# Kernel tuning notes

Hardware: AMD Instinct MI355X
Metric: run time of the kernel (lower is better)

Reference implementation:

```python
import jax, jax.numpy as jnp
import numpy as np

N_NODES = 50000
N_EDGES = 800000
D = 64
VOCAB = 1000
NUM_ITERS = 2
BN_EPS = 1e-5


def _bn(h, g, b):
    # BatchNorm1d in training mode: batch statistics over the edge dim, biased var
    mu = h.mean(axis=0)
    var = h.var(axis=0)
    return g * (h - mu) * jax.lax.rsqrt(var + BN_EPS) + b


def _edge_agg(x, idx_i, idx_j, W1, b1, g1, be1, W2, b2, g2, be2):
    # gather -> concat -> Linear+BN+ReLU x2 -> scatter-sum to idx_i -> degree norm
    m = jnp.concatenate([x[idx_i], x[idx_j]], axis=1)          # [E, 2D]
    h = jax.nn.relu(_bn(m @ W1 + b1, g1, be1))                  # [E, D]
    h = jax.nn.relu(_bn(h @ W2 + b2, g2, be2))                  # [E, D]
    agg = jax.ops.segment_sum(h, idx_i, num_segments=N_NODES)   # [N, D]
    deg = jax.ops.segment_sum(jnp.ones((idx_i.shape[0],), x.dtype), idx_i,
                              num_segments=N_NODES)
    deg_inv = jnp.where(deg > 0, 1.0 / deg, 0.0)
    return deg_inv[:, None] * agg


def setup_inputs() -> dict:
    key = jax.random.key(0)
    ks = jax.random.split(key, 24)
    s = 0.05
    inp = {
        'nodes': jax.random.randint(ks[0], (N_NODES,), 0, VOCAB),
        'edges': jax.random.randint(ks[1], (2, N_EDGES), 0, N_NODES),
        'emb': jax.random.normal(ks[2], (VOCAB, D), jnp.float32) * s,
        # parent aggregation MLP
        'p_W1': jax.random.normal(ks[3], (2 * D, D), jnp.float32) * s,
        'p_b1': jnp.zeros((D,), jnp.float32),
        'p_g1': jnp.ones((D,), jnp.float32),
        'p_be1': jnp.zeros((D,), jnp.float32),
        'p_W2': jax.random.normal(ks[4], (D, D), jnp.float32) * s,
        'p_b2': jnp.zeros((D,), jnp.float32),
        'p_g2': jnp.ones((D,), jnp.float32),
        'p_be2': jnp.zeros((D,), jnp.float32),
        # child aggregation MLP
        'c_W1': jax.random.normal(ks[5], (2 * D, D), jnp.float32) * s,
        'c_b1': jnp.zeros((D,), jnp.float32),
        'c_g1': jnp.ones((D,), jnp.float32),
        'c_be1': jnp.zeros((D,), jnp.float32),
        'c_W2': jax.random.normal(ks[6], (D, D), jnp.float32) * s,
        'c_b2': jnp.zeros((D,), jnp.float32),
        'c_g2': jnp.ones((D,), jnp.float32),
        'c_be2': jnp.zeros((D,), jnp.float32),
        # final aggregation (dropout = identity, eval semantics)
        'fc_W': jax.random.normal(ks[7], (3 * D, 2 * D), jnp.float32) * s,
        'fc_b': jnp.zeros((2 * D,), jnp.float32),
        'fc2_W': jax.random.normal(ks[8], (2 * D, D), jnp.float32) * s,
        'fc2_b': jnp.zeros((D,), jnp.float32),
        # Conv1d(D, 2D, kernel=1) == Linear D -> 2D
        'conv_W': jax.random.normal(ks[9], (D, 2 * D), jnp.float32) * s,
        'conv_b': jnp.zeros((2 * D,), jnp.float32),
    }
    return inp


def reference(nodes, edges, emb, p_W1, p_b1, p_g1, p_be1, p_W2, p_b2, p_g2, p_be2,
              c_W1, c_b1, c_g1, c_be1, c_W2, c_b2, c_g2, c_be2,
              fc_W, fc_b, fc2_W, fc2_b, conv_W, conv_b):
    src, dst = edges[0], edges[1]
    x = emb[nodes]                                            # [N, D]
    for _ in range(NUM_ITERS):
        # ParentAggregation: flow source_to_target -> x_i = x[dst], x_j = x[src], scatter to dst
        fi = _edge_agg(x, dst, src, p_W1, p_b1, p_g1, p_be1, p_W2, p_b2, p_g2, p_be2)
        # ChildAggregation: flow target_to_source -> x_i = x[src], x_j = x[dst], scatter to src
        fo = _edge_agg(x, src, dst, c_W1, c_b1, c_g1, c_be1, c_W2, c_b2, c_g2, c_be2)
        cat = jnp.concatenate([x, fi, fo], axis=1)            # [N, 3D]
        upd = jax.nn.relu(cat @ fc_W + fc_b) @ fc2_W + fc2_b  # [N, D]
        x = x + upd
    return x @ conv_W + conv_b                                # [N, 2D]
```

## Files before the change

kernel.cpp:

```cpp
#include <hip/hip_runtime.h>

#define NN 50000
#define NE 800000
#define BN_EPS 1e-5f
#define SCAN_T 256
#define SCAN_NB ((NN + SCAN_T - 1) / SCAN_T)

#define BKT_SH 8
#define NBKT ((NN + 255) >> 8)
#define CAP 6144
#define PCH 4096
#define NPB ((NE + PCH - 1) / PCH)

#define ST_SUM1 0
#define ST_SQ1 64
#define ST_CROSS 128
#define ST_SUM2 192
#define ST_SSQ2 256
#define ST_AGG 320

using bf16x8 = __attribute__((ext_vector_type(8))) __bf16;
using bf16x4 = __attribute__((ext_vector_type(4))) __bf16;
using floatx4 = __attribute__((ext_vector_type(4))) float;

// ... 131 lines not shown
      int u = (t >= o) ? sm[t - o] : 0;
      __syncthreads();
      sm[t] += u;
      __syncthreads();
    }
    if (t < SCAN_NB) btot[y * SCAN_NB + t] = sm[t] - v;
    __syncthreads();
  }
}

__global__ void k_scan3(const int* __restrict__ cnt_d, const int* __restrict__ cnt_s,
                        int* __restrict__ off_d, int* __restrict__ off_s,
                        const int* __restrict__ btot, float* __restrict__ dinv_d,
                        float* __restrict__ dinv_s) {
  const int* cnt = blockIdx.y ? cnt_s : cnt_d;
  int* off = blockIdx.y ? off_s : off_d;
  float* dinv = blockIdx.y ? dinv_s : dinv_d;
  int i = blockIdx.x * SCAN_T + threadIdx.x;
  if (i < NN) {
    int incl = off[i];
    int c = cnt[i];
    int o = incl - c + btot[blockIdx.y * SCAN_NB + blockIdx.x];
    off[i] = o;
    dinv[i] = c > 0 ? 1.0f / (float)c : 0.f;
  }
  if (i == NN - 1) off[NN] = NE;
}

__global__ void __launch_bounds__(256) k_fill2(const int* __restrict__ bcur,
                                               const unsigned int* __restrict__ stage,
                                               const int* __restrict__ off_d,
                                               const int* __restrict__ off_s,
                                               unsigned short* __restrict__ jl_d,
                                               unsigned short* __restrict__ jl_s) {
  const int dir = blockIdx.y;
  const int b = blockIdx.x;
  const int* off = dir ? off_s : off_d;
  unsigned short* jl = dir ? jl_s : jl_d;
  const unsigned int* st = stage + (size_t)dir * NBKT * CAP + (size_t)b * CAP;
  __shared__ int lcur[256];
  __shared__ unsigned short ljl[CAP];
  int csr0 = off[b << BKT_SH];
  int n = (b << BKT_SH) + threadIdx.x;
  lcur[threadIdx.x] = (n < NN) ? off[n] - csr0 : 0;
  __syncthreads();
  int sz = bcur[dir * NBKT + b] - b * CAP;
  for (int t = threadIdx.x; t < sz; t += 256) {
    unsigned int v = st[t];
    int p = atomicAdd(&lcur[(v >> 16) - (b << BKT_SH)], 1);
    ljl[p] = (unsigned short)(v & 0xFFFFu);
  }
  __syncthreads();
  for (int t = threadIdx.x; t < sz; t += 256) jl[csr0 + t] = ljl[t];
}

__global__ void __launch_bounds__(256) k_node_xform(
    const float* __restrict__ x, const float* __restrict__ W1,
    __bf16* __restrict__ Ab, __bf16* __restrict__ Bb,
    float* __restrict__ stats, int do_zero) {
  const int lane = threadIdx.x & 63;
  const int wid = threadIdx.x >> 6;
  __shared__ alignas(16) __bf16 xb[4][16 * 72];
  if (do_zero && blockIdx.x == 0)
    for (int t = threadIdx.x; t < 2 * ST_AGG; t += blockDim.x) stats[t] = 0.f;
  bf16x8 wfa[4][2], wfb[4][2];
#pragma unroll
  for (int ct = 0; ct < 4; ++ct)
#pragma unroll
    for (int kb = 0; kb < 2; ++kb) {
      wfa[ct][kb] = load_wfrag(W1, 64, kb, ct, lane);
      wfb[ct][kb] = load_wfrag(W1 + 64 * 64, 64, kb, ct, lane);
    }
  __bf16* vb = xb[wid];
  int wgid = (blockIdx.x * blockDim.x + threadIdx.x) >> 6;
  int nw = (gridDim.x * blockDim.x) >> 6;
  for (int tile = wgid; tile < NN / 16; tile += nw) {
#pragma unroll
    for (int t = 0; t < 16; ++t)
      vb[t * 72 + lane] = (__bf16)x[(tile * 16 + t) * 64 + lane];
    const bf16x8 a0 = *(const bf16x8*)&vb[(lane & 15) * 72 + ((lane >> 4) << 3)];
    const bf16x8 a1 = *(const bf16x8*)&vb[(lane & 15) * 72 + 32 + ((lane >> 4) << 3)];
#pragma unroll
    for (int ct = 0; ct < 4; ++ct) {
      floatx4 aA = {0.f, 0.f, 0.f, 0.f}, aB = {0.f, 0.f, 0.f, 0.f};
      aA = MFMA16(a0, wfa[ct][0], aA);
      aA = MFMA16(a1, wfa[ct][1], aA);
      aB = MFMA16(a0, wfb[ct][0], aB);
      aB = MFMA16(a1, wfb[ct][1], aB);
#pragma unroll
      for (int r = 0; r < 4; ++r) {
        int row = ((lane >> 4) << 2) + r;
        int o = (tile * 16 + row) * 64 + ct * 16 + (lane & 15);
        Ab[o] = (__bf16)aA[r];
        Bb[o] = (__bf16)aB[r];
      }
    }
  }
}

__global__ void __launch_bounds__(256) k_node_stats(
    const __bf16* __restrict__ Ap, const __bf16* __restrict__ Bp,
    const __bf16* __restrict__ Ac, const __bf16* __restrict__ Bc,
    const int* __restrict__ cnt_d, const int* __restrict__ cnt_s,
    float* __restrict__ stats) {
  const int lane = threadIdx.x & 63;
  const int g = lane >> 4, q = lane & 15;
  __shared__ float sacc[256];
  for (int t = threadIdx.x; t < 256; t += blockDim.x) sacc[t] = 0.f;
  __syncthreads();
  float sp[4] = {0, 0, 0, 0}, qp[4] = {0, 0, 0, 0};
  float sc[4] = {0, 0, 0, 0}, qc[4] = {0, 0, 0, 0};
  int wgid = (blockIdx.x * blockDim.x + threadIdx.x) >> 6;
  int nw = (gridDim.x * blockDim.x) >> 6;
  for (int ch = wgid; ch < NN / 4; ch += nw) {
    int n = ch * 4 + g;
    float wd = (float)cnt_d[n];
    float ws = (float)cnt_s[n];
    bf16x4 ap = *(const bf16x4*)(Ap + n * 64 + 4 * q);
    bf16x4 bp = *(const bf16x4*)(Bp + n * 64 + 4 * q);
    bf16x4 ac = *(const bf16x4*)(Ac + n * 64 + 4 * q);
    bf16x4 bc = *(const bf16x4*)(Bc + n * 64 + 4 * q);
#pragma unroll
    for (int k = 0; k < 4; ++k) {
      float a = (float)ap[k], b = (float)bp[k], c = (float)ac[k], d = (float)bc[k];
      sp[k] += wd * a + ws * b;
      qp[k] += wd * a * a + ws * b * b;
      sc[k] += ws * c + wd * d;
      qc[k] += ws * c * c + wd * d * d;
    }
  }
#pragma unroll
  for (int k = 0; k < 4; ++k) {
    sp[k] += __shfl_xor(sp[k], 16); sp[k] += __shfl_xor(sp[k], 32);
    qp[k] += __shfl_xor(qp[k], 16); qp[k] += __shfl_xor(qp[k], 32);
    sc[k] += __shfl_xor(sc[k], 16); sc[k] += __shfl_xor(sc[k], 32);
    qc[k] += __shfl_xor(qc[k], 16); qc[k] += __shfl_xor(qc[k], 32);
  }
  if (lane < 16) {
#pragma unroll
    for (int k = 0; k < 4; ++k) {
      atomicAdd(&sacc[4 * q + k], sp[k]);
      atomicAdd(&sacc[64 + 4 * q + k], qp[k]);
      atomicAdd(&sacc[128 + 4 * q + k], sc[k]);
      atomicAdd(&sacc[192 + 4 * q + k], qc[k]);
    }
  }
  __syncthreads();
  for (int t = threadIdx.x; t < 256; t += blockDim.x) {
    int dstoff = (t < 128) ? t : ST_AGG + (t - 128);
    atomicAdd(&stats[dstoff], sacc[t]);
  }
}

__global__ void __launch_bounds__(256) k_cross(
    const int* __restrict__ src, const int* __restrict__ dst,
    const __bf16* __restrict__ Ap, const __bf16* __restrict__ Bp,
    const __bf16* __restrict__ Ac, const __bf16* __restrict__ Bc,
    float* __restrict__ stats) {
  const int lane = threadIdx.x & 63;
  const int g = lane >> 4, q = lane & 15;
  __shared__ float sacc[128];
  for (int t = threadIdx.x; t < 128; t += blockDim.x) sacc[t] = 0.f;
  __syncthreads();
  float cp[4] = {0, 0, 0, 0}, cc[4] = {0, 0, 0, 0};
  int wgid = (blockIdx.x * blockDim.x + threadIdx.x) >> 6;
  int nw = (gridDim.x * blockDim.x) >> 6;
  for (int ch = wgid; ch < NE / 64; ch += nw) {
    int e0 = ch * 64;
    int s64 = src[e0 + lane];
    int d64 = dst[e0 + lane];
#pragma unroll 4
    for (int t = 0; t < 16; ++t) {
      int u = t * 4 + g;
      int s = __shfl(s64, u);
      int d = __shfl(d64, u);
      bf16x4 ap = *(const bf16x4*)(Ap + d * 64 + 4 * q);
      bf16x4 bp = *(const bf16x4*)(Bp + s * 64 + 4 * q);
      bf16x4 ac = *(const bf16x4*)(Ac + s * 64 + 4 * q);
      bf16x4 bc = *(const bf16x4*)(Bc + d * 64 + 4 * q);
#pragma unroll
      for (int k = 0; k < 4; ++k) {
        cp[k] += (float)ap[k] * (float)bp[k];
        cc[k] += (float)ac[k] * (float)bc[k];
      }
    }
  }
#pragma unroll
  for (int k = 0; k < 4; ++k) {
    cp[k] += __shfl_xor(cp[k], 16); cp[k] += __shfl_xor(cp[k], 32);
    cc[k] += __shfl_xor(cc[k], 16); cc[k] += __shfl_xor(cc[k], 32);
  }
  if (lane < 16) {
#pragma unroll
    for (int k = 0; k < 4; ++k) {
      atomicAdd(&sacc[4 * q + k], cp[k]);
      atomicAdd(&sacc[64 + 4 * q + k], cc[k]);
    }
  }
  __syncthreads();
  for (int t = threadIdx.x; t < 128; t += blockDim.x) {
    int dstoff = (t < 64) ? (ST_CROSS + t) : (ST_AGG + ST_CROSS + (t - 64));
    atomicAdd(&stats[dstoff], sacc[t]);
  }
}

__global__ void __launch_bounds__(256) k_edge_stats2(
    const int* __restrict__ src, const int* __restrict__ dst,
    const __bf16* __restrict__ Ap, const __bf16* __restrict__ Bp,
    const __bf16* __restrict__ Ac, const __bf16* __restrict__ Bc,
    const float* __restrict__ pg1, const float* __restrict__ pbe1,
    const float* __restrict__ cg1, const float* __restrict__ cbe1,
    const float* __restrict__ pW2, const float* __restrict__ cW2,
    float* __restrict__ stats) {
  const int lane = threadIdx.x & 63;
  const int wid = threadIdx.x >> 6;
  const int g = lane >> 4, q = lane & 15;
  __shared__ alignas(16) __bf16 vbuf[4][2][16 * 72];
  __shared__ float sred[256];
  float s1p[4], t1p[4], s1c[4], t1c[4];
#pragma unroll
  for (int k = 0; k < 4; ++k) {
    int c = 4 * q + k;
    float mu = stats[ST_SUM1 + c] * (1.f / NE);
    float var = (stats[ST_SQ1 + c] + 2.f * stats[ST_CROSS + c]) * (1.f / NE) - mu * mu;
    float s = pg1[c] * rsqrtf(var + BN_EPS);
    s1p[k] = s;
    t1p[k] = pbe1[c] - mu * s;
    mu = stats[ST_AGG + ST_SUM1 + c] * (1.f / NE);
    var = (stats[ST_AGG + ST_SQ1 + c] + 2.f * stats[ST_AGG + ST_CROSS + c]) * (1.f / NE) - mu * mu;
    s = cg1[c] * rsqrtf(var + BN_EPS);
    s1c[k] = s;
    t1c[k] = cbe1[c] - mu * s;
  }
  bf16x8 wfp[4][2], wfc[4][2];
#pragma unroll
  for (int ct = 0; ct < 4; ++ct)
#pragma unroll
    for (int kb = 0; kb < 2; ++kb) {
      wfp[ct][kb] = load_wfrag(pW2, 64, kb, ct, lane);
      wfc[ct][kb] = load_wfrag(cW2, 64, kb, ct, lane);
    }
  float sump[4] = {0, 0, 0, 0}, ssqp[4] = {0, 0, 0, 0};
  float sumc[4] = {0, 0, 0, 0}, ssqc[4] = {0, 0, 0, 0};
  __bf16* vbp = vbuf[wid][0];
  __bf16* vbc = vbuf[wid][1];
  int wgid = (blockIdx.x * blockDim.x + threadIdx.x) >> 6;
  int nw = (gridDim.x * blockDim.x) >> 6;
  for (int tile = wgid; tile < NE / 16; tile += nw) {
    int e0 = tile * 16;
    int s16 = src[e0 + q];
    int d16 = dst[e0 + q];
#pragma unroll
    for (int t = 0; t < 4; ++t) {
      int et = t * 4 + g;
      int s = __shfl(s16, et);
      int d = __shfl(d16, et);
      bf16x4 ap = *(const bf16x4*)(Ap + (size_t)d * 64 + 4 * q);
      bf16x4 bp = *(const bf16x4*)(Bp + (size_t)s * 64 + 4 * q);
      bf16x4 ac = *(const bf16x4*)(Ac + (size_t)s * 64 + 4 * q);
      bf16x4 bc = *(const bf16x4*)(Bc + (size_t)d * 64 + 4 * q);
      bf16x4 vp4, vc4;
#pragma unroll
      for (int k = 0; k < 4; ++k) {
        vp4[k] = (__bf16)fmaxf(s1p[k] * ((float)ap[k] + (float)bp[k]) + t1p[k], 0.f);
        vc4[k] = (__bf16)fmaxf(s1c[k] * ((float)ac[k] + (float)bc[k]) + t1c[k], 0.f);
      }
      *(bf16x4*)&vbp[et * 72 + 4 * q] = vp4;
      *(bf16x4*)&vbc[et * 72 + 4 * q] = vc4;
    }
    const bf16x8 a0p = *(const bf16x8*)&vbp[q * 72 + g * 8];
    const bf16x8 a1p = *(const bf16x8*)&vbp[q * 72 + 32 + g * 8];
    const bf16x8 a0c = *(const bf16x8*)&vbc[q * 72 + g * 8];
    const bf16x8 a1c = *(const bf16x8*)&vbc[q * 72 + 32 + g * 8];
#pragma unroll
    for (int ct = 0; ct < 4; ++ct) {
      floatx4 accp = {0.f, 0.f, 0.f, 0.f}, accc = {0.f, 0.f, 0.f, 0.f};
      accp = MFMA16(a0p, wfp[ct][0], accp);
      accp = MFMA16(a1p, wfp[ct][1], accp);
      accc = MFMA16(a0c, wfc[ct][0], accc);
      accc = MFMA16(a1c, wfc[ct][1], accc);
#pragma unroll
      for (int r = 0; r < 4; ++r) {
        float hp = accp[r], hc = accc[r];
        sump[ct] += hp;
        ssqp[ct] += hp * hp;
        sumc[ct] += hc;
        ssqc[ct] += hc * hc;
      }
    }
  }
  for (int t = threadIdx.x; t < 256; t += blockDim.x) sred[t] = 0.f;
  __syncthreads();
#pragma unroll
  for (int ct = 0; ct < 4; ++ct) {
    atomicAdd(&sred[ct * 16 + q], sump[ct]);
    atomicAdd(&sred[64 + ct * 16 + q], ssqp[ct]);
    atomicAdd(&sred[128 + ct * 16 + q], sumc[ct]);
    atomicAdd(&sred[192 + ct * 16 + q], ssqc[ct]);
  }
  __syncthreads();
  for (int t = threadIdx.x; t < 256; t += blockDim.x) {
    int dstoff;
    if (t < 64) dstoff = ST_SUM2 + t;
    else if (t < 128) dstoff = ST_SSQ2 + (t - 64);
    else if (t < 192) dstoff = ST_AGG + ST_SUM2 + (t - 128);
    else dstoff = ST_AGG + ST_SSQ2 + (t - 192);
    atomicAdd(&stats[dstoff], sred[t]);
  }
}

__global__ void __launch_bounds__(256) k_scatter_fused(
    const int* __restrict__ off, const float* __restrict__ dinv,
    const unsigned short* __restrict__ jl, const __bf16* __restrict__ A_,
    const __bf16* __restrict__ B_, const float* __restrict__ g1,
    const float* __restrict__ be1, const float* __restrict__ g2,
    const float* __restrict__ be2, const float* __restrict__ W2,
    const float* __restrict__ stats, int sbase, float* __restrict__ outb) {
  const int lane = threadIdx.x & 63;
  const int wid = threadIdx.x >> 6;
  const int g = lane >> 4, q = lane & 15;
  __shared__ alignas(16) __bf16 vbuf[4][16 * 72];
  float s1v[4], t1v[4];
#pragma unroll
  for (int k = 0; k < 4; ++k) {
    int c = 4 * q + k;
    float mu = stats[sbase + ST_SUM1 + c] * (1.f / NE);
    float var = (stats[sbase + ST_SQ1 + c] + 2.f * stats[sbase + ST_CROSS + c]) * (1.f / NE) - mu * mu;
    float s = g1[c] * rsqrtf(var + BN_EPS);
    s1v[k] = s;
    t1v[k] = be1[c] - mu * s;
  }
  float s2v[4], t2v[4];
#pragma unroll
  for (int ct = 0; ct < 4; ++ct) {
    int c = ct * 16 + q;
    float mu = stats[sbase + ST_SUM2 + c] * (1.f / NE);
    float var = stats[sbase + ST_SSQ2 + c] * (1.f / NE) - mu * mu;
    float s = g2[c] * rsqrtf(var + BN_EPS);
    s2v[ct] = s;
    t2v[ct] = be2[c] - mu * s;
  }
  bf16x8 wf[4][2];
#pragma unroll
  for (int ct = 0; ct < 4; ++ct)
#pragma unroll
    for (int kb = 0; kb < 2; ++kb) wf[ct][kb] = load_wfrag(W2, 64, kb, ct, lane);
  __bf16* vb = vbuf[wid];
  int wgid = (blockIdx.x * blockDim.x + threadIdx.x) >> 6;
  int nw = (gridDim.x * blockDim.x) >> 6;
  for (int n = wgid; n < NN; n += nw) {
    int p0 = off[n], p1 = off[n + 1];
    bf16x4 a4 = *(const bf16x4*)(A_ + (size_t)n * 64 + 4 * q);
    float ha[4];
#pragma unroll
    for (int k = 0; k < 4; ++k) ha[k] = (float)a4[k];
    float oacc[4] = {0.f, 0.f, 0.f, 0.f};
    for (int pt = p0; pt < p1; pt += 16) {
      int m = p1 - pt;
      if (m > 16) m = 16;
      int jj = (lane < m) ? (int)jl[pt + lane] : 0;
#pragma unroll
      for (int t = 0; t < 4; ++t) {
        int et = t * 4 + g;
        int j = __shfl(jj, et);
        bf16x4 b4 = *(const bf16x4*)(B_ + (size_t)j * 64 + 4 * q);
        bf16x4 v4;
#pragma unroll
        for (int k = 0; k < 4; ++k)
          v4[k] = (__bf16)fmaxf(s1v[k] * (ha[k] + (float)b4[k]) + t1v[k], 0.f);
        *(bf16x4*)&vb[et * 72 + 4 * q] = v4;
      }
      const bf16x8 a0 = *(const bf16x8*)&vb[q * 72 + g * 8];
      const bf16x8 a1 = *(const bf16x8*)&vb[q * 72 + 32 + g * 8];
#pragma unroll
      for (int ct = 0; ct < 4; ++ct) {
        floatx4 acc = {0.f, 0.f, 0.f, 0.f};
        acc = MFMA16(a0, wf[ct][0], acc);
        acc = MFMA16(a1, wf[ct][1], acc);
#pragma unroll
        for (int r = 0; r < 4; ++r)
          if (g * 4 + r < m) oacc[ct] += fmaxf(s2v[ct] * acc[r] + t2v[ct], 0.f);
      }
    }
#pragma unroll
    for (int ct = 0; ct < 4; ++ct) {
      oacc[ct] += __shfl_xor(oacc[ct], 16);
      oacc[ct] += __shfl_xor(oacc[ct], 32);
    }
    float val = (g == 0) ? oacc[0] : (g == 1) ? oacc[1] : (g == 2) ? oacc[2] : oacc[3];
    outb[(size_t)n * 64 + lane] = dinv[n] * val;
  }
}

__global__ void __launch_bounds__(256) k_node_update(
    float* __restrict__ x, const float* __restrict__ fi, const float* __restrict__ fo,
    const float* __restrict__ fcW, const float* __restrict__ fcb,
    const float* __restrict__ fc2W, const float* __restrict__ fc2b) {
  const int lane = threadIdx.x & 63;
  const int wid = threadIdx.x >> 6;
  __shared__ alignas(16) __bf16 cat[16 * 200];
  __shared__ alignas(16) __bf16 v2[16 * 136];
  bf16x8 wf1[2][6];
#pragma unroll
  for (int c = 0; c < 2; ++c) {
    int ct = 2 * wid + c;
#pragma unroll
    for (int kb = 0; kb < 6; ++kb) wf1[c][kb] = load_wfrag(fcW, 128, kb, ct, lane);
  }
  bf16x8 wf2[4];
#pragma unroll
  for (int kb = 0; kb < 4; ++kb) wf2[kb] = load_wfrag(fc2W, 64, kb, wid, lane);
  float fcbv[2];
#pragma unroll
  for (int c = 0; c < 2; ++c) fcbv[c] = fcb[(2 * wid + c) * 16 + (lane & 15)];
  float fc2bv = fc2b[wid * 16 + (lane & 15)];

  for (int tile = blockIdx.x; tile < NN / 16; tile += gridDim.x) {
#pragma unroll
    for (int r = 0; r < 4; ++r) {
      int rr = wid * 4 + r;
      int n = tile * 16 + rr;
      cat[rr * 200 + lane] = (__bf16)x[n * 64 + lane];
      cat[rr * 200 + 64 + lane] = (__bf16)fi[n * 64 + lane];
      cat[rr * 200 + 128 + lane] = (__bf16)fo[n * 64 + lane];
    }
    __syncthreads();
    floatx4 acc0 = {0.f, 0.f, 0.f, 0.f}, acc1 = {0.f, 0.f, 0.f, 0.f};
#pragma unroll
    for (int kb = 0; kb < 6; ++kb) {
      bf16x8 af = *(const bf16x8*)&cat[(lane & 15) * 200 + kb * 32 + ((lane >> 4) << 3)];
      acc0 = MFMA16(af, wf1[0][kb], acc0);
      acc1 = MFMA16(af, wf1[1][kb], acc1);
    }
#pragma unroll
    for (int r = 0; r < 4; ++r) {
      int row = ((lane >> 4) << 2) + r;
      v2[row * 136 + (2 * wid) * 16 + (lane & 15)] = (__bf16)fmaxf(acc0[r] + fcbv[0], 0.f);
      v2[row * 136 + (2 * wid + 1) * 16 + (lane & 15)] = (__bf16)fmaxf(acc1[r] + fcbv[1], 0.f);
    }
    __syncthreads();
    floatx4 a2 = {0.f, 0.f, 0.f, 0.f};
#pragma unroll
    for (int kb = 0; kb < 4; ++kb) {
      bf16x8 af = *(const bf16x8*)&v2[(lane & 15) * 136 + kb * 32 + ((lane >> 4) << 3)];
      a2 = MFMA16(af, wf2[kb], a2);
    }
#pragma unroll
    for (int r = 0; r < 4; ++r) {
      int row = ((lane >> 4) << 2) + r;
      int n = tile * 16 + row;
      x[n * 64 + wid * 16 + (lane & 15)] += a2[r] + fc2bv;
    }
    __syncthreads();
  }
}

__global__ void __launch_bounds__(256) k_conv(const float* __restrict__ x,
                                              const float* __restrict__ convW,
                                              const float* __restrict__ convb,
                                              float* __restrict__ out) {
  const int lane = threadIdx.x & 63;
  int wgid = (blockIdx.x * blockDim.x + threadIdx.x) >> 6;
  int nw = (gridDim.x * blockDim.x) >> 6;
  int half = wgid & 1;
  int col = half * 64 + lane;
  float wreg[64];
#pragma unroll
  for (int k = 0; k < 64; ++k) wreg[k] = convW[k * 128 + col];
  float bv = convb[col];
  for (int n = (wgid >> 1); n < NN; n += (nw >> 1)) {
    float xv = x[n * 64 + lane];
    float acc = bv;
#pragma unroll
    for (int k = 0; k < 64; ++k) acc += __shfl(xv, k) * wreg[k];
    out[(size_t)n * 128 + col] = acc;
  }
}

extern "C" void kernel_launch(void* const* d_in, const int* in_sizes, int n_in,
                              void* d_out, int out_size, void* d_ws, size_t ws_size,
                              hipStream_t stream) {
  const int* nodes = (const int*)d_in[0];
  const int* edges = (const int*)d_in[1];
  const int* src = edges;
  const int* dst = edges + NE;
  const float* emb = (const float*)d_in[2];
  const float* pW1 = (const float*)d_in[3];
  const float* pg1 = (const float*)d_in[5];
  const float* pbe1 = (const float*)d_in[6];
  const float* pW2 = (const float*)d_in[7];
  const float* pg2 = (const float*)d_in[9];
  const float* pbe2 = (const float*)d_in[10];
  const float* cW1 = (const float*)d_in[11];
  const float* cg1 = (const float*)d_in[13];
  const float* cbe1 = (const float*)d_in[14];
  const float* cW2 = (const float*)d_in[15];
  const float* cg2 = (const float*)d_in[17];
  const float* cbe2 = (const float*)d_in[18];
  const float* fcW = (const float*)d_in[19];
  const float* fcb = (const float*)d_in[20];
  const float* fc2W = (const float*)d_in[21];
  const float* fc2b = (const float*)d_in[22];
  const float* convW = (const float*)d_in[23];
  const float* convb = (const float*)d_in[24];
  float* out = (float*)d_out;

  char* w = (char*)d_ws;
  auto alloc = [&](size_t bytes) {
    char* p = w;
    w += (bytes + 255) & ~(size_t)255;
    return p;
  };
  float* x = (float*)alloc((size_t)NN * 64 * 4);
  __bf16* Ap = (__bf16*)alloc((size_t)NN * 64 * 2);
  __bf16* Bp = (__bf16*)alloc((size_t)NN * 64 * 2);
  __bf16* Ac = (__bf16*)alloc((size_t)NN * 64 * 2);
  __bf16* Bc = (__bf16*)alloc((size_t)NN * 64 * 2);
  float* fi = (float*)alloc((size_t)NN * 64 * 4);
  float* fo = (float*)alloc((size_t)NN * 64 * 4);
  unsigned short* jl_d = (unsigned short*)alloc((size_t)NE * 2);
  unsigned short* jl_s = (unsigned short*)alloc((size_t)NE * 2);
  int* off_d = (int*)alloc((size_t)(NN + 1) * 4);
  int* off_s = (int*)alloc((size_t)(NN + 1) * 4);
  int* cnt_d = (int*)alloc((size_t)NN * 4);
  int* cnt_s = (int*)alloc((size_t)NN * 4);
  float* dinv_d = (float*)alloc((size_t)NN * 4);
  float* dinv_s = (float*)alloc((size_t)NN * 4);
  float* stats = (float*)alloc(2 * ST_AGG * 4);
  int* btot = (int*)alloc(2 * SCAN_NB * 4);
  int* bcur = (int*)alloc((size_t)2 * NBKT * 4);
  unsigned int* stage = (unsigned int*)alloc((size_t)2 * NBKT * CAP * 4);

  k_setup<<<1024, 256, 0, stream>>>(nodes, emb, x, bcur);
  k_part<<<dim3(NPB, 2), 256, 0, stream>>>(src, dst, bcur, stage);
  k_count<<<dim3(NBKT, 2), 256, 0, stream>>>(bcur, stage, cnt_d, cnt_s);
  k_scan1<<<dim3(SCAN_NB, 2), SCAN_T, 0, stream>>>(cnt_d, cnt_s, off_d, off_s, btot);
  k_scan2<<<1, SCAN_T, 0, stream>>>(btot);
  k_scan3<<<dim3(SCAN_NB, 2), SCAN_T, 0, stream>>>(cnt_d, cnt_s, off_d, off_s, btot,
                                                   dinv_d, dinv_s);
  k_fill2<<<dim3(NBKT, 2), 256, 0, stream>>>(bcur, stage, off_d, off_s, jl_d, jl_s);

  for (int it = 0; it < 2; ++it) {
    k_node_xform<<<784, 256, 0, stream>>>(x, pW1, Ap, Bp, stats, 1);
    k_node_xform<<<784, 256, 0, stream>>>(x, cW1, Ac, Bc, stats, 0);
    k_node_stats<<<256, 256, 0, stream>>>(Ap, Bp, Ac, Bc, cnt_d, cnt_s, stats);
    k_cross<<<1024, 256, 0, stream>>>(src, dst, Ap, Bp, Ac, Bc, stats);
    k_edge_stats2<<<2048, 256, 0, stream>>>(src, dst, Ap, Bp, Ac, Bc, pg1, pbe1,
                                            cg1, cbe1, pW2, cW2, stats);
    k_scatter_fused<<<2048, 256, 0, stream>>>(off_d, dinv_d, jl_d, Ap, Bp, pg1, pbe1,
                                              pg2, pbe2, pW2, stats, 0, fi);
    k_scatter_fused<<<2048, 256, 0, stream>>>(off_s, dinv_s, jl_s, Ac, Bc, cg1, cbe1,
                                              cg2, cbe2, cW2, stats, ST_AGG, fo);
    k_node_update<<<3125, 256, 0, stream>>>(x, fi, fo, fcW, fcb, fc2W, fc2b);
  }
  k_conv<<<2048, 256, 0, stream>>>(x, convW, convb, out);
}
```

Before: 927.5 us.

## Materialize second-layer edge activations instead of recomputing them in the scatter pass

When the workspace is large enough, each aggregation direction now runs a CSR-ordered edge MLP kernel that computes layer-2 pre-BN activations once. It stores them in bf16 and accumulates their BN statistics, and a second kernel then applies BN2/ReLU and does the degree-normalized segment sum. This removes the old pattern where the stats pass and the scatter pass each recomputed the gather plus layer-2 matmul. In exchange it writes and reads a 100MB bf16 buffer per direction and adds bf16 rounding of pre-BN values. The old path is kept as a fallback when the workspace is too small.

Result: slower. 1.024 ms (+10.4%).

```diff
diff --git a/kernel.cpp b/kernel.cpp
--- a/kernel.cpp
+++ b/kernel.cpp
@@ -356,6 +356,141 @@
   for (int t = threadIdx.x; t < 128; t += blockDim.x) {
     int dstoff = (t < 64) ? (ST_CROSS + t) : (ST_AGG + ST_CROSS + (t - 64));
     atomicAdd(&stats[dstoff], sacc[t]);
+  }
+}
+
+__global__ void __launch_bounds__(256) k_edge_mlp(
+    const int* __restrict__ off, const unsigned short* __restrict__ jl,
+    const __bf16* __restrict__ A_, const __bf16* __restrict__ B_,
+    const float* __restrict__ g1, const float* __restrict__ be1,
+    const float* __restrict__ W2, float* __restrict__ stats, int sbase,
+    __bf16* __restrict__ hseq) {
+  const int lane = threadIdx.x & 63;
+  const int wid = threadIdx.x >> 6;
+  const int g = lane >> 4, q = lane & 15;
+  __shared__ alignas(16) __bf16 vbuf[4][16 * 72];
+  __shared__ float sred[128];
+  float s1v[4], t1v[4];
+#pragma unroll
+  for (int k = 0; k < 4; ++k) {
+    int c = 4 * q + k;
+    float mu = stats[sbase + ST_SUM1 + c] * (1.f / NE);
+    float var = (stats[sbase + ST_SQ1 + c] + 2.f * stats[sbase + ST_CROSS + c]) * (1.f / NE) - mu * mu;
+    float s = g1[c] * rsqrtf(var + BN_EPS);
+    s1v[k] = s;
+    t1v[k] = be1[c] - mu * s;
+  }
+  bf16x8 wf[4][2];
+#pragma unroll
+  for (int ct = 0; ct < 4; ++ct)
+#pragma unroll
+    for (int kb = 0; kb < 2; ++kb) wf[ct][kb] = load_wfrag(W2, 64, kb, ct, lane);
+  float sum2[4] = {0.f, 0.f, 0.f, 0.f}, ssq2[4] = {0.f, 0.f, 0.f, 0.f};
+  __bf16* vb = vbuf[wid];
+  int wgid = (blockIdx.x * blockDim.x + threadIdx.x) >> 6;
+  int nw = (gridDim.x * blockDim.x) >> 6;
+  for (int n = wgid; n < NN; n += nw) {
+    int p0 = off[n], p1 = off[n + 1];
+    bf16x4 a4 = *(const bf16x4*)(A_ + (size_t)n * 64 + 4 * q);
+    float ha[4];
+#pragma unroll
+    for (int k = 0; k < 4; ++k) ha[k] = (float)a4[k];
+    for (int pt = p0; pt < p1; pt += 16) {
+      int m = p1 - pt;
+      if (m > 16) m = 16;
+      int jj = (lane < m) ? (int)jl[pt + lane] : 0;
+#pragma unroll
+      for (int t = 0; t < 4; ++t) {
+        int et = t * 4 + g;
+        int j = __shfl(jj, et);
+        bf16x4 b4 = *(const bf16x4*)(B_ + (size_t)j * 64 + 4 * q);
+        bf16x4 v4;
+#pragma unroll
+        for (int k = 0; k < 4; ++k)
+          v4[k] = (__bf16)fmaxf(s1v[k] * (ha[k] + (float)b4[k]) + t1v[k], 0.f);
+        *(bf16x4*)&vb[et * 72 + 4 * q] = v4;
+      }
+      const bf16x8 a0 = *(const bf16x8*)&vb[q * 72 + g * 8];
+      const bf16x8 a1 = *(const bf16x8*)&vb[q * 72 + 32 + g * 8];
+      floatx4 acc[4];
+#pragma unroll
+      for (int ct = 0; ct < 4; ++ct) {
+        floatx4 a = {0.f, 0.f, 0.f, 0.f};
+        a = MFMA16(a0, wf[ct][0], a);
+        a = MFMA16(a1, wf[ct][1], a);
+        acc[ct] = a;
+      }
+#pragma unroll
+      for (int ct = 0; ct < 4; ++ct)
+#pragma unroll
+        for (int r = 0; r < 4; ++r) {
+          if (g * 4 + r < m) {
+            float h = acc[ct][r];
+            sum2[ct] += h;
+            ssq2[ct] += h * h;
+            hseq[(size_t)(pt + g * 4 + r) * 64 + ct * 16 + q] = (__bf16)h;
+          }
+        }
+    }
+  }
+  for (int t = threadIdx.x; t < 128; t += blockDim.x) sred[t] = 0.f;
+  __syncthreads();
+#pragma unroll
+  for (int ct = 0; ct < 4; ++ct) {
+    atomicAdd(&sred[ct * 16 + q], sum2[ct]);
+    atomicAdd(&sred[64 + ct * 16 + q], ssq2[ct]);
+  }
+  __syncthreads();
+  for (int t = threadIdx.x; t < 128; t += blockDim.x) {
+    int dstoff = (t < 64) ? (ST_SUM2 + t) : (ST_SSQ2 + (t - 64));
+    atomicAdd(&stats[sbase + dstoff], sred[t]);
+  }
+}
+
+__global__ void __launch_bounds__(256) k_bn2_apply(
+    const int* __restrict__ off, const float* __restrict__ dinv,
+    const __bf16* __restrict__ hseq, const float* __restrict__ g2,
+    const float* __restrict__ be2, const float* __restrict__ stats, int sbase,
+    float* __restrict__ outb) {
+  const int lane = threadIdx.x & 63;
+  const int c0 = (lane & 7) * 8;
+  float s2[8], t2[8];
+#pragma unroll
+  for (int j = 0; j < 8; ++j) {
+    int c = c0 + j;
+    float mu = stats[sbase + ST_SUM2 + c] * (1.f / NE);
+    float var = stats[sbase + ST_SSQ2 + c] * (1.f / NE) - mu * mu;
+    float s = g2[c] * rsqrtf(var + BN_EPS);
+    s2[j] = s;
+    t2[j] = be2[c] - mu * s;
+  }
+  int wgid = (blockIdx.x * blockDim.x + threadIdx.x) >> 6;
+  int nw = (gridDim.x * blockDim.x) >> 6;
+  for (int n = wgid; n < NN; n += nw) {
+    int p0 = off[n], p1 = off[n + 1];
+    float acc[8] = {0.f, 0.f, 0.f, 0.f, 0.f, 0.f, 0.f, 0.f};
+    for (int pt = p0; pt < p1; pt += 8) {
+      int r = pt + (lane >> 3);
+      if (r < p1) {
+        bf16x8 h = *(const bf16x8*)(hseq + (size_t)r * 64 + c0);
+#pragma unroll
+        for (int j = 0; j < 8; ++j)
+          acc[j] += fmaxf(s2[j] * (float)h[j] + t2[j], 0.f);
+      }
+    }
+#pragma unroll
+    for (int j = 0; j < 8; ++j) {
+      acc[j] += __shfl_xor(acc[j], 8);
+      acc[j] += __shfl_xor(acc[j], 16);
+      acc[j] += __shfl_xor(acc[j], 32);
+    }
+    if (lane < 8) {
+      float dv = dinv[n];
+      floatx4 o0 = {dv * acc[0], dv * acc[1], dv * acc[2], dv * acc[3]};
+      floatx4 o1 = {dv * acc[4], dv * acc[5], dv * acc[6], dv * acc[7]};
+      *(floatx4*)&outb[(size_t)n * 64 + lane * 8] = o0;
+      *(floatx4*)&outb[(size_t)n * 64 + lane * 8 + 4] = o1;
+    }
   }
 }
 
@@ -685,6 +820,8 @@
   int* btot = (int*)alloc(2 * SCAN_NB * 4);
   int* bcur = (int*)alloc((size_t)2 * NBKT * 4);
   unsigned int* stage = (unsigned int*)alloc((size_t)2 * NBKT * CAP * 4);
+  __bf16* hseq = (__bf16*)alloc((size_t)NE * 64 * 2);
+  const bool big_ws = ((size_t)(w - (char*)d_ws) <= ws_size);
 
   k_setup<<<1024, 256, 0, stream>>>(nodes, emb, x, bcur);
   k_part<<<dim3(NPB, 2), 256, 0, stream>>>(src, dst, bcur, stage);
@@ -700,12 +837,23 @@
     k_node_xform<<<784, 256, 0, stream>>>(x, cW1, Ac, Bc, stats, 0);
     k_node_stats<<<256, 256, 0, stream>>>(Ap, Bp, Ac, Bc, cnt_d, cnt_s, stats);
     k_cross<<<1024, 256, 0, stream>>>(src, dst, Ap, Bp, Ac, Bc, stats);
-    k_edge_stats2<<<2048, 256, 0, stream>>>(src, dst, Ap, Bp, Ac, Bc, pg1, pbe1,
-                                            cg1, cbe1, pW2, cW2, stats);
-    k_scatter_fused<<<2048, 256, 0, stream>>>(off_d, dinv_d, jl_d, Ap, Bp, pg1, pbe1,
-                                              pg2, pbe2, pW2, stats, 0, fi);
-    k_scatter_fused<<<2048, 256, 0, stream>>>(off_s, dinv_s, jl_s, Ac, Bc, cg1, cbe1,
-                                              cg2, cbe2, cW2, stats, ST_AGG, fo);
+    if (big_ws) {
+      k_edge_mlp<<<2048, 256, 0, stream>>>(off_d, jl_d, Ap, Bp, pg1, pbe1, pW2,
+                                           stats, 0, hseq);
+      k_bn2_apply<<<1024, 256, 0, stream>>>(off_d, dinv_d, hseq, pg2, pbe2, stats,
+                                            0, fi);
+      k_edge_mlp<<<2048, 256, 0, stream>>>(off_s, jl_s, Ac, Bc, cg1, cbe1, cW2,
+                                           stats, ST_AGG, hseq);
+      k_bn2_apply<<<1024, 256, 0, stream>>>(off_s, dinv_s, hseq, cg2, cbe2, stats,
+                                            ST_AGG, fo);
+    } else {
+      k_edge_stats2<<<2048, 256, 0, stream>>>(src, dst, Ap, Bp, Ac, Bc, pg1, pbe1,
+                                              cg1, cbe1, pW2, cW2, stats);
+      k_scatter_fused<<<2048, 256, 0, stream>>>(off_d, dinv_d, jl_d, Ap, Bp, pg1, pbe1,
+                                                pg2, pbe2, pW2, stats, 0, fi);
+      k_scatter_fused<<<2048, 256, 0, stream>>>(off_s, dinv_s, jl_s, Ac, Bc, cg1, cbe1,
+                                                cg2, cbe2, cW2, stats, ST_AGG, fo);
+    }
     k_node_update<<<3125, 256, 0, stream>>>(x, fi, fo, fcW, fcb, fc2W, fc2b);
   }
   k_conv<<<2048, 256, 0, stream>>>(x, convW, convb, out);
```

## Widen edge gathers to 16-byte loads and process two nodes per wave in scatter

Applied to the files above, without the earlier changes.

In the edge-stats and scatter kernels, each lane now gathers 8 bf16 values (16 bytes) of a row instead of 4, so 8 lanes cover a 64-wide row and one wave handles 8 edges per load step. The scatter kernel also processes two destination nodes per wave iteration, with separate LDS staging buffers and interleaved MFMAs. The goal is fewer, wider memory requests and more independent loads in flight to hide gather latency. The cost is higher register use, and when the two nodes have unequal degree the wave does masked work for the shorter one.

Result: no change. 939.3 us (+1.3%).

```diff
diff --git a/kernel.cpp b/kernel.cpp
--- a/kernel.cpp
+++ b/kernel.cpp
@@ -370,12 +370,14 @@
   const int lane = threadIdx.x & 63;
   const int wid = threadIdx.x >> 6;
   const int g = lane >> 4, q = lane & 15;
+  const int c8 = lane & 7;
+  const int e8 = lane >> 3;
   __shared__ alignas(16) __bf16 vbuf[4][2][16 * 72];
   __shared__ float sred[256];
-  float s1p[4], t1p[4], s1c[4], t1c[4];
-#pragma unroll
-  for (int k = 0; k < 4; ++k) {
-    int c = 4 * q + k;
+  float s1p[8], t1p[8], s1c[8], t1c[8];
+#pragma unroll
+  for (int k = 0; k < 8; ++k) {
+    int c = c8 * 8 + k;
     float mu = stats[ST_SUM1 + c] * (1.f / NE);
     float var = (stats[ST_SQ1 + c] + 2.f * stats[ST_CROSS + c]) * (1.f / NE) - mu * mu;
     float s = pg1[c] * rsqrtf(var + BN_EPS);
@@ -403,25 +405,25 @@
   int nw = (gridDim.x * blockDim.x) >> 6;
   for (int tile = wgid; tile < NE / 16; tile += nw) {
     int e0 = tile * 16;
-    int s16 = src[e0 + q];
-    int d16 = dst[e0 + q];
-#pragma unroll
-    for (int t = 0; t < 4; ++t) {
-      int et = t * 4 + g;
-      int s = __shfl(s16, et);
-      int d = __shfl(d16, et);
-      bf16x4 ap = *(const bf16x4*)(Ap + (size_t)d * 64 + 4 * q);
-      bf16x4 bp = *(const bf16x4*)(Bp + (size_t)s * 64 + 4 * q);
-      bf16x4 ac = *(const bf16x4*)(Ac + (size_t)s * 64 + 4 * q);
-      bf16x4 bc = *(const bf16x4*)(Bc + (size_t)d * 64 + 4 * q);
-      bf16x4 vp4, vc4;
-#pragma unroll
-      for (int k = 0; k < 4; ++k) {
-        vp4[k] = (__bf16)fmaxf(s1p[k] * ((float)ap[k] + (float)bp[k]) + t1p[k], 0.f);
-        vc4[k] = (__bf16)fmaxf(s1c[k] * ((float)ac[k] + (float)bc[k]) + t1c[k], 0.f);
+    int sv = src[e0 + q];
+    int dv = dst[e0 + q];
+#pragma unroll
+    for (int r = 0; r < 2; ++r) {
+      int ee = r * 8 + e8;
+      int s = __shfl(sv, ee);
+      int d = __shfl(dv, ee);
+      bf16x8 ap = *(const bf16x8*)(Ap + (size_t)d * 64 + c8 * 8);
+      bf16x8 bp = *(const bf16x8*)(Bp + (size_t)s * 64 + c8 * 8);
+      bf16x8 ac = *(const bf16x8*)(Ac + (size_t)s * 64 + c8 * 8);
+      bf16x8 bc = *(const bf16x8*)(Bc + (size_t)d * 64 + c8 * 8);
+      bf16x8 vp, vc;
+#pragma unroll
+      for (int k = 0; k < 8; ++k) {
+        vp[k] = (__bf16)fmaxf(s1p[k] * ((float)ap[k] + (float)bp[k]) + t1p[k], 0.f);
+        vc[k] = (__bf16)fmaxf(s1c[k] * ((float)ac[k] + (float)bc[k]) + t1c[k], 0.f);
       }
-      *(bf16x4*)&vbp[et * 72 + 4 * q] = vp4;
-      *(bf16x4*)&vbc[et * 72 + 4 * q] = vc4;
+      *(bf16x8*)&vbp[ee * 72 + c8 * 8] = vp;
+      *(bf16x8*)&vbc[ee * 72 + c8 * 8] = vc;
     }
     const bf16x8 a0p = *(const bf16x8*)&vbp[q * 72 + g * 8];
     const bf16x8 a1p = *(const bf16x8*)&vbp[q * 72 + 32 + g * 8];
@@ -474,11 +476,13 @@
   const int lane = threadIdx.x & 63;
   const int wid = threadIdx.x >> 6;
   const int g = lane >> 4, q = lane & 15;
-  __shared__ alignas(16) __bf16 vbuf[4][16 * 72];
-  float s1v[4], t1v[4];
-#pragma unroll
-  for (int k = 0; k < 4; ++k) {
-    int c = 4 * q + k;
+  const int c8 = lane & 7;
+  const int e8 = lane >> 3;
+  __shared__ alignas(16) __bf16 vbuf[4][2][16 * 72];
+  float s1v[8], t1v[8];
+#pragma unroll
+  for (int k = 0; k < 8; ++k) {
+    int c = c8 * 8 + k;
     float mu = stats[sbase + ST_SUM1 + c] * (1.f / NE);
     float var = (stats[sbase + ST_SQ1 + c] + 2.f * stats[sbase + ST_CROSS + c]) * (1.f / NE) - mu * mu;
     float s = g1[c] * rsqrtf(var + BN_EPS);
@@ -500,50 +504,77 @@
   for (int ct = 0; ct < 4; ++ct)
 #pragma unroll
     for (int kb = 0; kb < 2; ++kb) wf[ct][kb] = load_wfrag(W2, 64, kb, ct, lane);
-  __bf16* vb = vbuf[wid];
+  __bf16* vb0 = vbuf[wid][0];
+  __bf16* vb1 = vbuf[wid][1];
   int wgid = (blockIdx.x * blockDim.x + threadIdx.x) >> 6;
   int nw = (gridDim.x * blockDim.x) >> 6;
-  for (int n = wgid; n < NN; n += nw) {
-    int p0 = off[n], p1 = off[n + 1];
-    bf16x4 a4 = *(const bf16x4*)(A_ + (size_t)n * 64 + 4 * q);
-    float ha[4];
-#pragma unroll
-    for (int k = 0; k < 4; ++k) ha[k] = (float)a4[k];
-    float oacc[4] = {0.f, 0.f, 0.f, 0.f};
-    for (int pt = p0; pt < p1; pt += 16) {
-      int m = p1 - pt;
-      if (m > 16) m = 16;
-      int jj = (lane < m) ? (int)jl[pt + lane] : 0;
-#pragma unroll
-      for (int t = 0; t < 4; ++t) {
-        int et = t * 4 + g;
-        int j = __shfl(jj, et);
-        bf16x4 b4 = *(const bf16x4*)(B_ + (size_t)j * 64 + 4 * q);
-        bf16x4 v4;
-#pragma unroll
-        for (int k = 0; k < 4; ++k)
-          v4[k] = (__bf16)fmaxf(s1v[k] * (ha[k] + (float)b4[k]) + t1v[k], 0.f);
-        *(bf16x4*)&vb[et * 72 + 4 * q] = v4;
+  for (int pp = wgid; pp < NN / 2; pp += nw) {
+    int n0 = 2 * pp, n1 = n0 + 1;
+    int p00 = off[n0], p01 = off[n1], p11 = off[n1 + 1];
+    int d0 = p01 - p00, d1 = p11 - p01;
+    bf16x8 a80 = *(const bf16x8*)(A_ + (size_t)n0 * 64 + c8 * 8);
+    bf16x8 a81 = *(const bf16x8*)(A_ + (size_t)n1 * 64 + c8 * 8);
+    float ha0[8], ha1[8];
+#pragma unroll
+    for (int k = 0; k < 8; ++k) { ha0[k] = (float)a80[k]; ha1[k] = (float)a81[k]; }
+    float oacc0[4] = {0.f, 0.f, 0.f, 0.f};
+    float oacc1[4] = {0.f, 0.f, 0.f, 0.f};
+    int T0 = (d0 + 15) >> 4, T1 = (d1 + 15) >> 4;
+    int T = (T0 > T1) ? T0 : T1;
+    for (int tt = 0; tt < T; ++tt) {
+      int b = tt * 16;
+      int m0 = d0 - b; if (m0 > 16) m0 = 16;
+      int m1 = d1 - b; if (m1 > 16) m1 = 16;
+      int jj0 = (lane < m0) ? (int)jl[p00 + b + lane] : 0;
+      int jj1 = (lane < m1) ? (int)jl[p01 + b + lane] : 0;
+      int j00 = __shfl(jj0, e8), j01 = __shfl(jj0, 8 + e8);
+      int j10 = __shfl(jj1, e8), j11 = __shfl(jj1, 8 + e8);
+      bf16x8 b00 = *(const bf16x8*)(B_ + (size_t)j00 * 64 + c8 * 8);
+      bf16x8 b01 = *(const bf16x8*)(B_ + (size_t)j01 * 64 + c8 * 8);
+      bf16x8 b10 = *(const bf16x8*)(B_ + (size_t)j10 * 64 + c8 * 8);
+      bf16x8 b11 = *(const bf16x8*)(B_ + (size_t)j11 * 64 + c8 * 8);
+      bf16x8 w00, w01, w10, w11;
+#pragma unroll
+      for (int k = 0; k < 8; ++k) {
+        w00[k] = (__bf16)fmaxf(s1v[k] * (ha0[k] + (float)b00[k]) + t1v[k], 0.f);
+        w01[k] = (__bf16)fmaxf(s1v[k] * (ha0[k] + (float)b01[k]) + t1v[k], 0.f);
+        w10[k] = (__bf16)fmaxf(s1v[k] * (ha1[k] + (float)b10[k]) + t1v[k], 0.f);
+        w11[k] = (__bf16)fmaxf(s1v[k] * (ha1[k] + (float)b11[k]) + t1v[k], 0.f);
       }
-      const bf16x8 a0 = *(const bf16x8*)&vb[q * 72 + g * 8];
-      const bf16x8 a1 = *(const bf16x8*)&vb[q * 72 + 32 + g * 8];
+      *(bf16x8*)&vb0[e8 * 72 + c8 * 8] = w00;
+      *(bf16x8*)&vb0[(8 + e8) * 72 + c8 * 8] = w01;
+      *(bf16x8*)&vb1[e8 * 72 + c8 * 8] = w10;
+      *(bf16x8*)&vb1[(8 + e8) * 72 + c8 * 8] = w11;
+      const bf16x8 f00 = *(const bf16x8*)&vb0[q * 72 + g * 8];
+      const bf16x8 f01 = *(const bf16x8*)&vb0[q * 72 + 32 + g * 8];
+      const bf16x8 f10 = *(const bf16x8*)&vb1[q * 72 + g * 8];
+      const bf16x8 f11 = *(const bf16x8*)&vb1[q * 72 + 32 + g * 8];
 #pragma unroll
       for (int ct = 0; ct < 4; ++ct) {
-        floatx4 acc = {0.f, 0.f, 0.f, 0.f};
-        acc = MFMA16(a0, wf[ct][0], acc);
-        acc = MFMA16(a1, wf[ct][1], acc);
-#pragma unroll
-        for (int r = 0; r < 4; ++r)
-          if (g * 4 + r < m) oacc[ct] += fmaxf(s2v[ct] * acc[r] + t2v[ct], 0.f);
+        floatx4 acc0 = {0.f, 0.f, 0.f, 0.f};
+        acc0 = MFMA16(f00, wf[ct][0], acc0);
+        acc0 = MFMA16(f01, wf[ct][1], acc0);
+        floatx4 acc1 = {0.f, 0.f, 0.f, 0.f};
+        acc1 = MFMA16(f10, wf[ct][0], acc1);
+        acc1 = MFMA16(f11, wf[ct][1], acc1);
+#pragma unroll
+        for (int r = 0; r < 4; ++r) {
+          if (g * 4 + r < m0) oacc0[ct] += fmaxf(s2v[ct] * acc0[r] + t2v[ct], 0.f);
+          if (g * 4 + r < m1) oacc1[ct] += fmaxf(s2v[ct] * acc1[r] + t2v[ct], 0.f);
+        }
       }
     }
 #pragma unroll
     for (int ct = 0; ct < 4; ++ct) {
-      oacc[ct] += __shfl_xor(oacc[ct], 16);
-      oacc[ct] += __shfl_xor(oacc[ct], 32);
-    }
-    float val = (g == 0) ? oacc[0] : (g == 1) ? oacc[1] : (g == 2) ? oacc[2] : oacc[3];
-    outb[(size_t)n * 64 + lane] = dinv[n] * val;
+      oacc0[ct] += __shfl_xor(oacc0[ct], 16);
+      oacc0[ct] += __shfl_xor(oacc0[ct], 32);
+      oacc1[ct] += __shfl_xor(oacc1[ct], 16);
+      oacc1[ct] += __shfl_xor(oacc1[ct], 32);
+    }
+    float v0 = (g == 0) ? oacc0[0] : (g == 1) ? oacc0[1] : (g == 2) ? oacc0[2] : oacc0[3];
+    float v1 = (g == 0) ? oacc1[0] : (g == 1) ? oacc1[1] : (g == 2) ? oacc1[2] : oacc1[3];
+    outb[(size_t)n0 * 64 + lane] = dinv[n0] * v0;
+    outb[(size_t)n1 * 64 + lane] = dinv[n1] * v1;
   }
 }
 
```

## Iterate edge statistics kernels over dst-sorted CSR to reuse per-node rows

Applied to the files above, without the earlier changes.

The cross-term and second-layer BN statistics kernels now walk the dst-grouped CSR (off_d, jl_d) instead of the raw src/dst edge list. Each wavefront owns one destination node, loads its Ap/Bc rows once into registers, and gathers only the neighbour Bp/Ac rows using 16-byte loads, with 8 lanes per row. This removes half of the random row gathers and the per-edge index reads. The cost is warp divergence and idle lanes on low-degree nodes, because partial 16-edge tiles are padded with zeros before the MFMA.

Result: slower. 1.003 ms (+8.2%).

```diff
diff --git a/kernel.cpp b/kernel.cpp
--- a/kernel.cpp
+++ b/kernel.cpp
@@ -307,49 +307,63 @@
   }
 }
 
-__global__ void __launch_bounds__(256) k_cross(
-    const int* __restrict__ src, const int* __restrict__ dst,
+__global__ void __launch_bounds__(256) k_cross_csr(
+    const int* __restrict__ off, const unsigned short* __restrict__ jl,
     const __bf16* __restrict__ Ap, const __bf16* __restrict__ Bp,
     const __bf16* __restrict__ Ac, const __bf16* __restrict__ Bc,
     float* __restrict__ stats) {
   const int lane = threadIdx.x & 63;
-  const int g = lane >> 4, q = lane & 15;
+  const int c8 = lane & 7, e4 = lane >> 3;
   __shared__ float sacc[128];
   for (int t = threadIdx.x; t < 128; t += blockDim.x) sacc[t] = 0.f;
   __syncthreads();
-  float cp[4] = {0, 0, 0, 0}, cc[4] = {0, 0, 0, 0};
+  float cp[8] = {0, 0, 0, 0, 0, 0, 0, 0}, cc[8] = {0, 0, 0, 0, 0, 0, 0, 0};
   int wgid = (blockIdx.x * blockDim.x + threadIdx.x) >> 6;
   int nw = (gridDim.x * blockDim.x) >> 6;
-  for (int ch = wgid; ch < NE / 64; ch += nw) {
-    int e0 = ch * 64;
-    int s64 = src[e0 + lane];
-    int d64 = dst[e0 + lane];
-#pragma unroll 4
-    for (int t = 0; t < 16; ++t) {
-      int u = t * 4 + g;
-      int s = __shfl(s64, u);
-      int d = __shfl(d64, u);
-      bf16x4 ap = *(const bf16x4*)(Ap + d * 64 + 4 * q);
-      bf16x4 bp = *(const bf16x4*)(Bp + s * 64 + 4 * q);
-      bf16x4 ac = *(const bf16x4*)(Ac + s * 64 + 4 * q);
-      bf16x4 bc = *(const bf16x4*)(Bc + d * 64 + 4 * q);
-#pragma unroll
-      for (int k = 0; k < 4; ++k) {
-        cp[k] += (float)ap[k] * (float)bp[k];
-        cc[k] += (float)ac[k] * (float)bc[k];
+  for (int n = wgid; n < NN; n += nw) {
+    int p0 = off[n], p1 = off[n + 1];
+    if (p0 == p1) continue;
+    bf16x8 ap8 = *(const bf16x8*)(Ap + (size_t)n * 64 + c8 * 8);
+    bf16x8 bc8 = *(const bf16x8*)(Bc + (size_t)n * 64 + c8 * 8);
+    float apf[8], bcf[8];
+#pragma unroll
+    for (int k = 0; k < 8; ++k) { apf[k] = (float)ap8[k]; bcf[k] = (float)bc8[k]; }
+    for (int pt = p0; pt < p1; pt += 16) {
+      int m = p1 - pt;
+      if (m > 16) m = 16;
+      int jj = (lane < m) ? (int)jl[pt + lane] : 0;
+      int ja = __shfl(jj, e4);
+      int jb = __shfl(jj, 8 + e4);
+      bf16x8 bpa = *(const bf16x8*)(Bp + (size_t)ja * 64 + c8 * 8);
+      bf16x8 aca = *(const bf16x8*)(Ac + (size_t)ja * 64 + c8 * 8);
+      bf16x8 bpb = *(const bf16x8*)(Bp + (size_t)jb * 64 + c8 * 8);
+      bf16x8 acb = *(const bf16x8*)(Ac + (size_t)jb * 64 + c8 * 8);
+      if (e4 < m) {
+#pragma unroll
+        for (int k = 0; k < 8; ++k) {
+          cp[k] += apf[k] * (float)bpa[k];
+          cc[k] += bcf[k] * (float)aca[k];
+        }
       }
-    }
-  }
-#pragma unroll
-  for (int k = 0; k < 4; ++k) {
-    cp[k] += __shfl_xor(cp[k], 16); cp[k] += __shfl_xor(cp[k], 32);
-    cc[k] += __shfl_xor(cc[k], 16); cc[k] += __shfl_xor(cc[k], 32);
-  }
-  if (lane < 16) {
-#pragma unroll
-    for (int k = 0; k < 4; ++k) {
-      atomicAdd(&sacc[4 * q + k], cp[k]);
-      atomicAdd(&sacc[64 + 4 * q + k], cc[k]);
+      if (8 + e4 < m) {
+#pragma unroll
+        for (int k = 0; k < 8; ++k) {
+          cp[k] += apf[k] * (float)bpb[k];
+          cc[k] += bcf[k] * (float)acb[k];
+        }
+      }
+    }
+  }
+#pragma unroll
+  for (int k = 0; k < 8; ++k) {
+    cp[k] += __shfl_xor(cp[k], 8);  cp[k] += __shfl_xor(cp[k], 16); cp[k] += __shfl_xor(cp[k], 32);
+    cc[k] += __shfl_xor(cc[k], 8);  cc[k] += __shfl_xor(cc[k], 16); cc[k] += __shfl_xor(cc[k], 32);
+  }
+  if (lane < 8) {
+#pragma unroll
+    for (int k = 0; k < 8; ++k) {
+      atomicAdd(&sacc[c8 * 8 + k], cp[k]);
+      atomicAdd(&sacc[64 + c8 * 8 + k], cc[k]);
     }
   }
   __syncthreads();
@@ -359,8 +373,8 @@
   }
 }
 
-__global__ void __launch_bounds__(256) k_edge_stats2(
-    const int* __restrict__ src, const int* __restrict__ dst,
+__global__ void __launch_bounds__(256) k_edge_stats_csr(
+    const int* __restrict__ off, const unsigned short* __restrict__ jl,
     const __bf16* __restrict__ Ap, const __bf16* __restrict__ Bp,
     const __bf16* __restrict__ Ac, const __bf16* __restrict__ Bc,
     const float* __restrict__ pg1, const float* __restrict__ pbe1,
@@ -370,12 +384,13 @@
   const int lane = threadIdx.x & 63;
   const int wid = threadIdx.x >> 6;
   const int g = lane >> 4, q = lane & 15;
+  const int c8 = lane & 7, e8 = lane >> 3;
   __shared__ alignas(16) __bf16 vbuf[4][2][16 * 72];
   __shared__ float sred[256];
-  float s1p[4], t1p[4], s1c[4], t1c[4];
-#pragma unroll
-  for (int k = 0; k < 4; ++k) {
-    int c = 4 * q + k;
+  float s1p[8], t1p[8], s1c[8], t1c[8];
+#pragma unroll
+  for (int k = 0; k < 8; ++k) {
+    int c = c8 * 8 + k;
     float mu = stats[ST_SUM1 + c] * (1.f / NE);
     float var = (stats[ST_SQ1 + c] + 2.f * stats[ST_CROSS + c]) * (1.f / NE) - mu * mu;
     float s = pg1[c] * rsqrtf(var + BN_EPS);
@@ -401,46 +416,53 @@
   __bf16* vbc = vbuf[wid][1];
   int wgid = (blockIdx.x * blockDim.x + threadIdx.x) >> 6;
   int nw = (gridDim.x * blockDim.x) >> 6;
-  for (int tile = wgid; tile < NE / 16; tile += nw) {
-    int e0 = tile * 16;
-    int s16 = src[e0 + q];
-    int d16 = dst[e0 + q];
-#pragma unroll
-    for (int t = 0; t < 4; ++t) {
-      int et = t * 4 + g;
-      int s = __shfl(s16, et);
-      int d = __shfl(d16, et);
-      bf16x4 ap = *(const bf16x4*)(Ap + (size_t)d * 64 + 4 * q);
-      bf16x4 bp = *(const bf16x4*)(Bp + (size_t)s * 64 + 4 * q);
-      bf16x4 ac = *(const bf16x4*)(Ac + (size_t)s * 64 + 4 * q);
-      bf16x4 bc = *(const bf16x4*)(Bc + (size_t)d * 64 + 4 * q);
-      bf16x4 vp4, vc4;
-#pragma unroll
-      for (int k = 0; k < 4; ++k) {
-        vp4[k] = (__bf16)fmaxf(s1p[k] * ((float)ap[k] + (float)bp[k]) + t1p[k], 0.f);
-        vc4[k] = (__bf16)fmaxf(s1c[k] * ((float)ac[k] + (float)bc[k]) + t1c[k], 0.f);
+  for (int n = wgid; n < NN; n += nw) {
+    int p0 = off[n], p1 = off[n + 1];
+    if (p0 == p1) continue;
+    bf16x8 ap8 = *(const bf16x8*)(Ap + (size_t)n * 64 + c8 * 8);
+    bf16x8 bc8 = *(const bf16x8*)(Bc + (size_t)n * 64 + c8 * 8);
+    float hap[8], hbc[8];
+#pragma unroll
+    for (int k = 0; k < 8; ++k) { hap[k] = (float)ap8[k]; hbc[k] = (float)bc8[k]; }
+    for (int pt = p0; pt < p1; pt += 16) {
+      int m = p1 - pt;
+      if (m > 16) m = 16;
+      int jj = (lane < m) ? (int)jl[pt + lane] : 0;
+#pragma unroll
+      for (int r = 0; r < 2; ++r) {
+        int ee = r * 8 + e8;
+        int j = __shfl(jj, ee);
+        bf16x8 bp = *(const bf16x8*)(Bp + (size_t)j * 64 + c8 * 8);
+        bf16x8 ac = *(const bf16x8*)(Ac + (size_t)j * 64 + c8 * 8);
+        bf16x8 vp, vc;
+        bool valid = (ee < m);
+#pragma unroll
+        for (int k = 0; k < 8; ++k) {
+          vp[k] = valid ? (__bf16)fmaxf(s1p[k] * (hap[k] + (float)bp[k]) + t1p[k], 0.f) : (__bf16)0.f;
+          vc[k] = valid ? (__bf16)fmaxf(s1c[k] * ((float)ac[k] + hbc[k]) + t1c[k], 0.f) : (__bf16)0.f;
+        }
+        *(bf16x8*)&vbp[ee * 72 + c8 * 8] = vp;
+        *(bf16x8*)&vbc[ee * 72 + c8 * 8] = vc;
       }
-      *(bf16x4*)&vbp[et * 72 + 4 * q] = vp4;
-      *(bf16x4*)&vbc[et * 72 + 4 * q] = vc4;
-    }
-    const bf16x8 a0p = *(const bf16x8*)&vbp[q * 72 + g * 8];
-    const bf16x8 a1p = *(const bf16x8*)&vbp[q * 72 + 32 + g * 8];
-    const bf16x8 a0c = *(const bf16x8*)&vbc[q * 72 + g * 8];
-    const bf16x8 a1c = *(const bf16x8*)&vbc[q * 72 + 32 + g * 8];
-#pragma unroll
-    for (int ct = 0; ct < 4; ++ct) {
-      floatx4 accp = {0.f, 0.f, 0.f, 0.f}, accc = {0.f, 0.f, 0.f, 0.f};
-      accp = MFMA16(a0p, wfp[ct][0], accp);
-      accp = MFMA16(a1p, wfp[ct][1], accp);
-      accc = MFMA16(a0c, wfc[ct][0], accc);
-      accc = MFMA16(a1c, wfc[ct][1], accc);
-#pragma unroll
-      for (int r = 0; r < 4; ++r) {
-        float hp = accp[r], hc = accc[r];
-        sump[ct] += hp;
-        ssqp[ct] += hp * hp;
-        sumc[ct] += hc;
-        ssqc[ct] += hc * hc;
+      const bf16x8 a0p = *(const bf16x8*)&vbp[q * 72 + g * 8];
+      const bf16x8 a1p = *(const bf16x8*)&vbp[q * 72 + 32 + g * 8];
+      const bf16x8 a0c = *(const bf16x8*)&vbc[q * 72 + g * 8];
+      const bf16x8 a1c = *(const bf16x8*)&vbc[q * 72 + 32 + g * 8];
+#pragma unroll
+      for (int ct = 0; ct < 4; ++ct) {
+        floatx4 accp = {0.f, 0.f, 0.f, 0.f}, accc = {0.f, 0.f, 0.f, 0.f};
+        accp = MFMA16(a0p, wfp[ct][0], accp);
+        accp = MFMA16(a1p, wfp[ct][1], accp);
+        accc = MFMA16(a0c, wfc[ct][0], accc);
+        accc = MFMA16(a1c, wfc[ct][1], accc);
+#pragma unroll
+        for (int r = 0; r < 4; ++r) {
+          float hp = accp[r], hc = accc[r];
+          sump[ct] += hp;
+          ssqp[ct] += hp * hp;
+          sumc[ct] += hc;
+          ssqc[ct] += hc * hc;
+        }
       }
     }
   }
@@ -699,9 +721,9 @@
     k_node_xform<<<784, 256, 0, stream>>>(x, pW1, Ap, Bp, stats, 1);
     k_node_xform<<<784, 256, 0, stream>>>(x, cW1, Ac, Bc, stats, 0);
     k_node_stats<<<256, 256, 0, stream>>>(Ap, Bp, Ac, Bc, cnt_d, cnt_s, stats);
-    k_cross<<<1024, 256, 0, stream>>>(src, dst, Ap, Bp, Ac, Bc, stats);
-    k_edge_stats2<<<2048, 256, 0, stream>>>(src, dst, Ap, Bp, Ac, Bc, pg1, pbe1,
-                                            cg1, cbe1, pW2, cW2, stats);
+    k_cross_csr<<<2048, 256, 0, stream>>>(off_d, jl_d, Ap, Bp, Ac, Bc, stats);
+    k_edge_stats_csr<<<2048, 256, 0, stream>>>(off_d, jl_d, Ap, Bp, Ac, Bc, pg1, pbe1,
+                                               cg1, cbe1, pW2, cW2, stats);
     k_scatter_fused<<<2048, 256, 0, stream>>>(off_d, dinv_d, jl_d, Ap, Bp, pg1, pbe1,
                                               pg2, pbe2, pW2, stats, 0, fi);
     k_scatter_fused<<<2048, 256, 0, stream>>>(off_s, dinv_s, jl_s, Ac, Bc, cg1, cbe1,
```
